# Performance work log

Measured on AMD Instinct MI355X. Metric: run time of the kernel, lower is better.

The kernel has to match this reference:

```python
import jax, jax.numpy as jnp
import numpy as np

B, N, D = 2, 2048, 1536
HEADS, KVH, DQK, DV = 8, 1, 128, 192
G = HEADS // KVH  # query groups per kv head
NP, DP = 512, 128  # pairwise seq len (coarse), pairwise feature dim
SCALE = DQK ** -0.5
CLAMP = 5.0
MOMENTUM = 0.1  # BatchRMSNorm: 1 - 0.9
EPS = 1e-5


def layernorm(x, w, b):
    mu = jnp.mean(x, axis=-1, keepdims=True)
    var = jnp.mean(jnp.square(x - mu), axis=-1, keepdims=True)
    return (x - mu) * jax.lax.rsqrt(var + EPS) * w + b


def setup_inputs() -> dict:
    key = jax.random.key(0)
    ks = jax.random.split(key, 6)
    w = lambda k, shape: jax.random.normal(k, shape, jnp.float32) * 0.02
    return {
        "x": jax.random.normal(ks[0], (B, N, D), jnp.float32),
        "pairwise": jax.random.normal(ks[1], (B, NP, NP, DP), jnp.float32),
        "w_qkv": w(ks[2], (D, HEADS * DQK + KVH * DQK + KVH * DV)),
        "q_w": jnp.ones((DQK,), jnp.float32), "q_b": jnp.zeros((DQK,), jnp.float32),
        "k_w": jnp.ones((DQK,), jnp.float32), "k_b": jnp.zeros((DQK,), jnp.float32),
        "v_w": jnp.ones((DV,), jnp.float32), "v_b": jnp.zeros((DV,), jnp.float32),
        "bias_gamma": jnp.ones((DP,), jnp.float32),
        "bias_beta": jnp.zeros((DP,), jnp.float32),
        "bias_running_var": jnp.ones((DP,), jnp.float32),
        "w_bias": w(ks[3], (DP, HEADS)),
        "w_out": w(ks[4], (HEADS * DV, D)),
        "b_out": jnp.zeros((D,), jnp.float32),
    }


def reference(x, pairwise, w_qkv, q_w, q_b, k_w, k_b, v_w, v_b,
              bias_gamma, bias_beta, bias_running_var, w_bias, w_out, b_out):
    b, n, _ = x.shape
    qkv = x @ w_qkv
    q, k, v = jnp.split(qkv, [HEADS * DQK, HEADS * DQK + KVH * DQK], axis=-1)
    # split heads: q -> b g h n d, k/v -> b h n d
    q = q.reshape(b, n, G, KVH, DQK).transpose(0, 2, 3, 1, 4)
    k = k.reshape(b, n, KVH, DQK).transpose(0, 2, 1, 3)
    v = v.reshape(b, n, KVH, DV).transpose(0, 2, 1, 3)
    q = layernorm(q, q_w, q_b)
    k = layernorm(k, k_w, k_b)
    v = layernorm(v, v_w, v_b)

    sim = jnp.einsum('bghid,bhjd->bghij', q, k) * SCALE

    # BatchRMSNorm (training update of running_var, then normalize)
    flat = pairwise.reshape(-1, DP)
    batch_var = jnp.var(flat, axis=0)  # unbiased=False
    rv = bias_running_var * (1.0 - MOMENTUM) + MOMENTUM * batch_var
    std = jnp.sqrt(rv + EPS)
    normed = pairwise / std * bias_gamma + bias_beta
    bias = jax.nn.gelu(normed, approximate=False) @ w_bias  # b i j (g h)
    bias = bias.reshape(b, NP, NP, G, KVH).transpose(0, 3, 4, 1, 2)  # b g h i j
    r = n // NP  # expand_factor
    bias = jnp.repeat(jnp.repeat(bias, r, axis=-2), r, axis=-1)

    sim = jnp.tanh((sim + bias) / CLAMP) * CLAMP  # softclamp
    attn = jax.nn.softmax(sim, axis=-1)
    out = jnp.einsum('bghij,bhjd->bghid', attn, v)
    out = out.transpose(0, 3, 1, 2, 4).reshape(b, n, HEADS * DV)  # merge heads
    return out @ w_out + b_out
```

## Files before the change

### kernel.cpp

```cpp
#include <hip/hip_runtime.h>
#include <math.h>

typedef _Float16 f16;
typedef unsigned int u32;
typedef __attribute__((ext_vector_type(8))) f16 f16x8;
typedef __attribute__((ext_vector_type(4))) f16 f16x4;
typedef __attribute__((ext_vector_type(4))) float f32x4;
typedef __attribute__((ext_vector_type(16))) float f32x16;

#define DEV static __device__ __forceinline__

#define SEQ 2048
#define DMODEL 1536
#define NHEADS 8
#define DQK 128
#define DVV 192
#define QKVW 1344
#define SCALEQK 0.08838834764831845f
#define LOG2E 1.4426950408889634f

#define OFF_WQKVT 0ull
#define OFF_WOUTT 4128768ull
#define OFF_XH    8847360ull
#define OFF_QKV   21430272ull
#define OFF_Q     43450368ull
#define OFF_K     51838976ull
#define OFF_V     52887552ull
#define OFF_VT    54460416ull
#define OFF_PART  56033280ull
#define OFF_SG    57081856ull
#define OFF_BIASC 57082880ull
#define OFF_AO    65471488ull

DEV float fexp2(float x){
#if __has_builtin(__builtin_amdgcn_exp2f)
  return __builtin_amdgcn_exp2f(x);
#else
  return exp2f(x);
#endif
}
DEV float frcp(float x){
#if __has_builtin(__builtin_amdgcn_rcpf)
  return __builtin_amdgcn_rcpf(x);
#else
  return 1.0f/x;
#endif
}

typedef u32 __attribute__((address_space(1))) u32g;
typedef u32 __attribute__((address_space(3))) u32l;
DEV void g2l16(const void* g, void* l){
  __builtin_amdgcn_global_load_lds((const u32g*)g, (u32l*)l, 16, 0, 0);
}

#define MFMA32(a,b,c) __builtin_amdgcn_mfma_f32_32x32x16_f16(a,b,c,0,0,0)
#define MFMA16(a,b,c) __builtin_amdgcn_mfma_f32_16x16x32_f16(a,b,c,0,0,0)

DEV f32x16 zero16(){
  f32x16 v;
  #pragma unroll
  for (int i=0;i<16;i++) v[i]=0.f;
  return v;
}
DEV f32x4 zero4(){
  f32x4 v;
  #pragma unroll
  for (int i=0;i<4;i++) v[i]=0.f;
  return v;
}

DEV float gelu_f(float x){
  float z  = 0.70710678118654752440f * x;
  float az = fabsf(z);
  float t  = frcp(1.f + 0.3275911f*az);
  float poly = t*(0.254829592f + t*(-0.284496736f + t*(1.421413741f +
               t*(-1.453152027f + t*1.061405429f))));
  float e  = 1.f - poly*fexp2(-z*z*LOG2E);
  float er = (z < 0.f) ? -e : e;
  return 0.5f*x*(1.f + er);
}

__global__ __launch_bounds__(256) void k1_prep(const float* __restrict__ wq, f16* __restrict__ wqT,
                                               const float* __restrict__ wo, f16* __restrict__ woT,
                                               const float* __restrict__ X, f16* __restrict__ Xh){
  __shared__ float t[32][33];
  int bid = blockIdx.x, tid = threadIdx.x;
  if (bid >= 4320){
    size_t i0 = (size_t)(bid - 4320)*2048 + (size_t)tid*8;
    f32x4 a = *(const f32x4*)(X + i0);
    f32x4 b = *(const f32x4*)(X + i0 + 4);
    f16x8 o;
    #pragma unroll
    for (int e=0;e<4;e++){ o[e] = (f16)a[e]; o[4+e] = (f16)b[e]; }
    *(f16x8*)(Xh + i0) = o;
    return;
  }
  int tx = tid & 31, ty = tid >> 5;
  const float* src; f16* dst; int N, x, y;
  if (bid < 2016){ src = wq; dst = wqT; N = 1344; x = bid % 48; y = bid / 48; }
  else { int b2 = bid - 2016; src = wo; dst = woT; N = 1536; x = b2 % 48; y = b2 / 48; }
  int k0 = x*32, n0 = y*32;
  #pragma unroll
  for (int i=0;i<4;i++){ int r = ty+8*i; t[r][tx] = src[(size_t)(k0+r)*N + n0+tx]; }
  __syncthreads();
  #pragma unroll
  for (int i=0;i<4;i++){ int r = ty+8*i; dst[(size_t)(n0+r)*1536 + k0+tx] = (f16)t[tx][r]; }
}

DEV void qkv_body(const f16* __restrict__ A, const f16* __restrict__ WT,
                  float* __restrict__ qkv, char* lds, int bx, int by, int tid){
  int nb = bx*64, mb = by*128;
  int w = tid>>6, lane = tid&63, li = lane&31, h = lane>>5;
  int srow = lane>>3, sc = lane&7;
  f32x16 acc[2]; acc[0]=zero16(); acc[1]=zero16();

#define QG_STAGE(buf, kt_) do { \
    char* ad = lds + (buf)*24576; \
    _Pragma("unroll") \
    for (int s=0;s<4;s++){ \
      int slot = w*4+s; int mlr = slot*8 + srow; int cs = sc ^ (mlr&7); \
      g2l16(A + (size_t)(mb+mlr)*DMODEL + (kt_)*64 + cs*8, ad + slot*1024); \
    } \
    char* bd = lds + (buf)*24576 + 16384; \
    _Pragma("unroll") \
    for (int s=0;s<2;s++){ \
      int slot = w*2+s; int nl = slot*8 + srow; int cs = sc ^ (nl&7); \
      g2l16(WT + (size_t)(nb+nl)*DMODEL + (kt_)*64 + cs*8, bd + slot*1024); \
    } } while(0)

  QG_STAGE(0,0);
  __syncthreads();
  for (int kt=0; kt<24; kt++){
    int cur = kt&1;
    if (kt<23) QG_STAGE(cur^1, kt+1);
    const char* ad = lds + cur*24576;
    const char* bd = lds + cur*24576 + 16384;
    int ml = w*32 + li;
    #pragma unroll
    for (int ks=0; ks<4; ks++){
      f16x8 af = *(const f16x8*)(ad + ml*128 + (((2*ks+h) ^ (ml&7))*16));
      #pragma unroll
      for (int nf=0; nf<2; nf++){
        int nl = nf*32 + li;
        f16x8 bf = *(const f16x8*)(bd + nl*128 + (((2*ks+h) ^ (nl&7))*16));
        acc[nf] = MFMA32(af, bf, acc[nf]);
      }
    }
    __syncthreads();
  }
  #pragma unroll
  for (int nf=0; nf<2; nf++)
    #pragma unroll
    for (int r=0;r<16;r++){
      int m = mb + w*32 + (r&3) + 8*(r>>2) + 4*h;
      int n = nb + nf*32 + li;
      qkv[(size_t)m*QKVW + n] = acc[nf][r];
    }
#undef QG_STAGE
}

DEV void pvar_body(const float* __restrict__ pw, float* __restrict__ partials,
                   char* smem, int id, int tid){
  int q = tid & 31, rg = tid >> 5;
  f32x4 s1 = zero4(), s2 = zero4();
  const float* p0 = pw + ((size_t)id*512 + rg)*128 + q*4;
  #pragma unroll 4
  for (int it=0; it<64; it++){
    f32x4 v = *(const f32x4*)(p0 + (size_t)it*1024);
    s1 += v; s2 += v*v;
  }
  f32x4* r1 = (f32x4*)smem; f32x4* r2 = r1 + 256;
  r1[tid] = s1; r2[tid] = s2;
  __syncthreads();
  if (tid < 64){
    int qq = tid & 31;
    f32x4* rr = (tid >= 32) ? r2 : r1;
    f32x4 a = rr[qq];
    #pragma unroll
    for (int g=1; g<8; g++) a += rr[g*32+qq];
    *(f32x4*)(partials + (size_t)id*256 + ((tid>=32)?128:0) + qq*4) = a;
  }
}

__global__ __launch_bounds__(256,2) void k2_qkv_pvar(const f16* __restrict__ Xh,
    const f16* __restrict__ WT, float* __restrict__ qkv,
    const float* __restrict__ pw, float* __restrict__ partials){
  __shared__ char smem[49152];
  int bid = blockIdx.x, tid = threadIdx.x;
  if (bid < 1536){
    if (bid % 3 == 0){ int qid = bid/3; qkv_body(Xh, WT, qkv, smem, qid%21, qid/21, tid); }
    else { int pid = (bid/3)*2 + (bid%3) - 1; pvar_body(pw, partials, smem, pid, tid); }
  } else {
    int qid = 512 + (bid - 1536);
    qkv_body(Xh, WT, qkv, smem, qid%21, qid/21, tid);
  }
}

DEV void ln_unit(const float* __restrict__ qkv,
    const float* __restrict__ qw, const float* __restrict__ qb,
    const float* __restrict__ kw, const float* __restrict__ kb,
    const float* __restrict__ vw, const float* __restrict__ vb,
    f16* __restrict__ Q, f16* __restrict__ K, f16* __restrict__ V,
    int unit, int lane){
  int row = unit / 10, seg = unit - row*10;
  int b = row >> 11, n = row & 2047;
  const float* base = qkv + (size_t)row*QKVW;
  if (seg < 9){
    int off = seg*128;
    float x0 = base[off+lane], x1 = base[off+64+lane];
    float s = x0+x1;
    #pragma unroll
    for (int d=32; d>=1; d>>=1) s += __shfl_xor(s, d);
    float mu = s*(1.f/128.f);
    float d0 = x0-mu, d1 = x1-mu;
    float vv = d0*d0 + d1*d1;
    #pragma unroll
    for (int d=32; d>=1; d>>=1) vv += __shfl_xor(vv, d);
    float istd = rsqrtf(vv*(1.f/128.f) + 1e-5f);
    const float* W  = (seg<8)? qw : kw;
    const float* Bi = (seg<8)? qb : kb;
    f16* dst = (seg<8) ? (Q + ((size_t)(b*NHEADS+seg)*SEQ + n)*DQK)
                       : (K + ((size_t)(b*SEQ+n))*DQK);
    dst[lane]    = (f16)(d0*istd*W[lane] + Bi[lane]);
    dst[lane+64] = (f16)(d1*istd*W[lane+64] + Bi[lane+64]);
  } else {
    float x0 = base[1152+lane], x1 = base[1152+64+lane], x2 = base[1152+128+lane];
    float s = x0+x1+x2;
    #pragma unroll
    for (int d=32; d>=1; d>>=1) s += __shfl_xor(s, d);
    float mu = s*(1.f/192.f);
    float d0=x0-mu, d1=x1-mu, d2=x2-mu;
    float vv = d0*d0+d1*d1+d2*d2;
    #pragma unroll
    for (int d=32; d>=1; d>>=1) vv += __shfl_xor(vv, d);
    float istd = rsqrtf(vv*(1.f/192.f) + 1e-5f);
    f16* dst = V + (size_t)(b*SEQ+n)*DVV;
    dst[lane]     = (f16)(d0*istd*vw[lane] + vb[lane]);
    dst[lane+64]  = (f16)(d1*istd*vw[lane+64] + vb[lane+64]);
    dst[lane+128] = (f16)(d2*istd*vw[lane+128] + vb[lane+128]);
  }
}

__global__ __launch_bounds__(256,4) void k3_ln_finvar(const float* __restrict__ qkv,
    const float* __restrict__ qw, const float* __restrict__ qb,
    const float* __restrict__ kw, const float* __restrict__ kb,
    const float* __restrict__ vw, const float* __restrict__ vb,
    f16* __restrict__ Q, f16* __restrict__ K, f16* __restrict__ V,
    const float* __restrict__ partials, const float* __restrict__ rvar,
    const float* __restrict__ gamma, const float* __restrict__ beta,
    float* __restrict__ sg, float* __restrict__ sb){
  __shared__ float sh[256];
  int bid = blockIdx.x, tid = threadIdx.x;
  if (bid < 10240){
    ln_unit(qkv, qw,qb,kw,kb,vw,vb, Q,K,V, bid*4 + (tid>>6), tid&63);
  } else {
    int c = tid & 127, wh = tid >> 7;
    float acc = 0.f;
    #pragma unroll 8
    for (int i=0;i<1024;i++) acc += partials[i*256 + wh*128 + c];
    sh[tid] = acc;
    __syncthreads();
    if (tid < 128){
      float s1 = sh[tid], s2 = sh[tid+128];
      const float Minv = 1.f/524288.f;
      float m = s1*Minv;
      float var = s2*Minv - m*m;
      float rv = rvar[tid]*0.9f + 0.1f*var;
      sg[tid] = rsqrtf(rv + 1e-5f)*gamma[tid];
      sb[tid] = beta[tid];
    }
  }
}

DEV void bias_body(const float* __restrict__ pw,
    const float* __restrict__ sg, const float* __restrict__ sb,
    const float* __restrict__ wb, f16* __restrict__ biasc, int bias_id, int tid){
  int w = tid>>6, lane = tid&63;
  int il = lane&15, kg = lane>>4;
  f16x8 bw[4];
  float sgr[32], sbr[32];
  #pragma unroll
  for (int t=0;t<4;t++)
    #pragma unroll
    for (int e=0;e<8;e++){
      int k = t*32 + kg*8 + e;
      bw[t][e] = (f16)((il<8) ? wb[k*8 + il] : 0.f);
      sgr[t*8+e] = sg[k];
      sbr[t*8+e] = sb[k];
    }
  for (int it=0; it<8; it++){
    int tile = bias_id*4 + w + it*4096;
    size_t rg = (size_t)tile*16 + il;
    f32x4 acc = zero4();
    #pragma unroll
    for (int t=0;t<4;t++){
      const float* sp = pw + rg*128 + t*32 + kg*8;
      f32x4 v0 = *(const f32x4*)sp;
      f32x4 v1 = *(const f32x4*)(sp+4);
      f16x8 af;
      #pragma unroll
      for (int e=0;e<4;e++) af[e]   = (f16)gelu_f(v0[e]*sgr[t*8+e]   + sbr[t*8+e]);
      #pragma unroll
      for (int e=0;e<4;e++) af[4+e] = (f16)gelu_f(v1[e]*sgr[t*8+4+e] + sbr[t*8+4+e]);
      acc = MFMA16(af, bw[t], acc);
    }
    if (il < 8){
      #pragma unroll
      for (int r=0;r<4;r++){
        size_t rr = (size_t)tile*16 + kg*4 + r;
        int bb = (int)(rr >> 18);
        int rem = (int)(rr & 262143);
        int ii = rem >> 9, jj = rem & 511;
        biasc[(((size_t)(bb*8 + il)*512) + ii)*512 + jj] = (f16)acc[r];
      }
    }
  }
}

DEV void vtrans_body(const f16* __restrict__ V, f16* __restrict__ VT,
                     f16 (*t)[33], int id, int tid){
  int b = id / 384, rem = id - b*384;
  int d0 = (rem % 6)*32, j0 = (rem / 6)*32;
  int tx = tid & 31, ty = tid >> 5;
  #pragma unroll
  for (int i=0;i<4;i++){ int r = ty+8*i; t[r][tx] = V[((size_t)b*SEQ + j0+r)*DVV + d0+tx]; }
  __syncthreads();
  #pragma unroll
  for (int i=0;i<4;i++){ int r = ty+8*i; VT[((size_t)b*DVV + d0+r)*SEQ + j0+tx] = t[tx][r]; }
}

__global__ __launch_bounds__(256,2) void k4_bias_vtrans(const float* __restrict__ pw,
    const float* __restrict__ sg, const float* __restrict__ sb,
    const float* __restrict__ wb, f16* __restrict__ biasc,
    const f16* __restrict__ V, f16* __restrict__ VT){
  __shared__ f16 tt[32][33];
  int bid = blockIdx.x, tid = threadIdx.x;
  if (bid < 1536){
    if (bid & 1) bias_body(pw, sg, sb, wb, biasc, bid>>1, tid);
    else         vtrans_body(V, VT, tt, bid>>1, tid);
  } else {
    bias_body(pw, sg, sb, wb, biasc, 768 + (bid - 1536), tid);
  }
}

__global__ __launch_bounds__(256,1) void attn(const f16* __restrict__ Q, const f16* __restrict__ K,
                                              const f16* __restrict__ VT, const f16* __restrict__ biasc,
                                              f16* __restrict__ AO){
  __shared__ char lds[81920];
  int bid = blockIdx.x;
  int bg = bid & 15, qt = bid >> 4;
  int b = bg >> 3, g = bg & 7;
  int tid = threadIdx.x;
  int w = tid >> 6, lane = tid & 63;
  int li = lane & 31, h = lane >> 5;

  const f16* Qb = Q  + (size_t)bg*SEQ*DQK;
  const f16* Kb = K  + (size_t)b*SEQ*DQK;
  const f16* Vb = VT + (size_t)b*DVV*SEQ;

  int qrow = qt*128 + w*32 + li;
  f16x8 qf[8];
  #pragma unroll
  for (int ks=0; ks<8; ks++)
    qf[ks] = *(const f16x8*)(Qb + (size_t)qrow*DQK + ks*16 + h*8);

  const f16* brow = biasc + ((size_t)bg*512 + (qrow>>2))*512;

  f32x16 oacc[6];
  #pragma unroll
  for (int nf=0;nf<6;nf++) oacc[nf] = zero16();
  float lsum = 0.f;

  int kl_row = lane >> 4, kl_c = lane & 15;
  int vl_row = lane >> 3, vl_c = lane & 7;

#define STAGE(buf, jt_) do { \
    char* kd = lds + (buf)*40960; \
    const f16* ksrc = Kb + (size_t)(jt_)*64*DQK; \
    _Pragma("unroll") \
    for (int s=0;s<4;s++){ \
      int slot = w*4+s; int jr = slot*4 + kl_row; int cs = kl_c ^ (jr&7); \
      g2l16(ksrc + (size_t)jr*DQK + cs*8, kd + slot*1024); \
    } \
    char* vd = lds + (buf)*40960 + 16384; \
    _Pragma("unroll") \
    for (int s=0;s<6;s++){ \
      int slot = w*6+s; int dvr = slot*8 + vl_row; int cs = vl_c ^ (dvr&7); \
      g2l16(Vb + (size_t)dvr*SEQ + (size_t)(jt_)*64 + cs*8, vd + slot*1024); \
    } } while(0)

  STAGE(0, 0);

  const float CS = SCALEQK * (2.f*LOG2E/5.f);
  const float CB = 2.f*LOG2E/5.f;
  const float CP = 5.f*LOG2E;

  for (int jt=0; jt<32; jt++){
    int cur = jt & 1;
    __syncthreads();
    if (jt < 31) STAGE(cur^1, jt+1);
    const char* kb_ = lds + cur*40960;
    const char* vb_ = lds + cur*40960 + 16384;
    #pragma unroll
    for (int sub=0; sub<2; sub++){
      f32x16 sacc = zero16();
      int jr = sub*32 + li;
      #pragma unroll
      for (int ks=0; ks<8; ks++){
        int ck = (2*ks + h) ^ (jr&7);
        f16x8 kf = *(const f16x8*)(kb_ + jr*256 + ck*16);
        sacc = MFMA32(kf, qf[ks], sacc);
      }
      int jb4 = jt*16 + sub*8;
      f16x8 bv = *(const f16x8*)(brow + jb4);
      float bt[4];
      #pragma unroll
      for (int q=0;q<4;q++){
        float b0 = (float)bv[2*q], b1 = (float)bv[2*q+1];
        bt[q] = (h ? b1 : b0) * CB;
      }
      float p[16], xp[16];
      #pragma unroll
      for (int r=0;r<16;r++){
        float u2 = sacc[r]*CS + bt[r>>2];
        float E  = fexp2(u2);
        float tn = 1.f - 2.f*frcp(E + 1.f);
        float pr = fexp2(tn * CP);
        p[r] = pr;
        lsum += pr;
      }
      #pragma unroll
      for (int r=0;r<16;r++) xp[r] = __shfl_xor(p[r], 32);
      #pragma unroll
      for (int ks2=0; ks2<2; ks2++){
        f16x8 pa;
        #pragma unroll
        for (int e=0;e<4;e++) pa[e] = (f16)(h ? xp[8*ks2+4+e] : p[8*ks2+e]);
        #pragma unroll
        for (int e=4;e<8;e++) pa[e] = (f16)(h ? p[8*ks2+e]    : xp[8*ks2+e-4]);
        #pragma unroll
        for (int nf=0; nf<6; nf++){
          int dvr = nf*32 + li;
          int cj = (sub*4 + 2*ks2 + h) ^ (dvr&7);
          f16x8 vf = *(const f16x8*)(vb_ + dvr*128 + cj*16);
          oacc[nf] = MFMA32(pa, vf, oacc[nf]);
        }
      }
    }
  }
  float ltot = lsum + __shfl_xor(lsum, 32);
  float linv = 1.f / ltot;
  #pragma unroll
  for (int nf=0; nf<6; nf++)
    #pragma unroll
    for (int r=0;r<16;r++){
      int il = (r&3) + 8*(r>>2) + 4*h;
      float ov = oacc[nf][r] * __shfl(linv, il);
      int orow = qt*128 + w*32 + il;
      AO[((size_t)(b*SEQ + orow)*NHEADS + g)*DVV + nf*32 + li] = (f16)ov;
    }
#undef STAGE
}

__global__ __launch_bounds__(256,2) void out_gemm(const f16* __restrict__ A, const f16* __restrict__ WT,
                                                  const float* __restrict__ bo, float* __restrict__ out){
  __shared__ char lds[49152];
  int nb = blockIdx.x*64, mb = blockIdx.y*128;
  int tid = threadIdx.x;
  int w = tid>>6, lane = tid&63, li = lane&31, h = lane>>5;
  int srow = lane>>3, sc = lane&7;
  f32x16 acc[2]; acc[0]=zero16(); acc[1]=zero16();

#define OG_STAGE(buf, kt_) do { \
    char* ad = lds + (buf)*24576; \
    _Pragma("unroll") \
    for (int s=0;s<4;s++){ \
      int slot = w*4+s; int mlr = slot*8 + srow; int cs = sc ^ (mlr&7); \
      g2l16(A + (size_t)(mb+mlr)*DMODEL + (kt_)*64 + cs*8, ad + slot*1024); \
    } \
    char* bd = lds + (buf)*24576 + 16384; \
    _Pragma("unroll") \
    for (int s=0;s<2;s++){ \
      int slot = w*2+s; int nl = slot*8 + srow; int cs = sc ^ (nl&7); \
      g2l16(WT + (size_t)(nb+nl)*DMODEL + (kt_)*64 + cs*8, bd + slot*1024); \
    } } while(0)

  OG_STAGE(0,0);
  __syncthreads();
  for (int kt=0; kt<24; kt++){
    int cur = kt&1;
    if (kt<23) OG_STAGE(cur^1, kt+1);
    const char* ad = lds + cur*24576;
    const char* bd = lds + cur*24576 + 16384;
    int ml = w*32 + li;
    #pragma unroll
    for (int ks=0; ks<4; ks++){
      f16x8 af = *(const f16x8*)(ad + ml*128 + (((2*ks+h) ^ (ml&7))*16));
      #pragma unroll
      for (int nf=0; nf<2; nf++){
        int nl = nf*32 + li;
        f16x8 bf = *(const f16x8*)(bd + nl*128 + (((2*ks+h) ^ (nl&7))*16));
        acc[nf] = MFMA32(af, bf, acc[nf]);
      }
    }
    __syncthreads();
  }
  float bo0 = bo[nb+li], bo1 = bo[nb+32+li];
  #pragma unroll
  for (int nf=0; nf<2; nf++)
    #pragma unroll
    for (int r=0;r<16;r++){
      int m = mb + w*32 + (r&3) + 8*(r>>2) + 4*h;
      int n = nb + nf*32 + li;
      out[(size_t)m*DMODEL + n] = acc[nf][r] + (nf ? bo1 : bo0);
    }
#undef OG_STAGE
}

extern "C" void kernel_launch(void* const* d_in, const int* in_sizes, int n_in,
                              void* d_out, int out_size, void* d_ws, size_t ws_size,
                              hipStream_t stream) {
  (void)in_sizes; (void)n_in; (void)out_size; (void)ws_size;
  const float* x        = (const float*)d_in[0];
  const float* pairwise = (const float*)d_in[1];
  const float* w_qkv    = (const float*)d_in[2];
  const float* q_w      = (const float*)d_in[3];
  const float* q_b      = (const float*)d_in[4];
  const float* k_w      = (const float*)d_in[5];
  const float* k_b      = (const float*)d_in[6];
  const float* v_w      = (const float*)d_in[7];
  const float* v_b      = (const float*)d_in[8];
  const float* bgamma   = (const float*)d_in[9];
  const float* bbeta    = (const float*)d_in[10];
  const float* brvar    = (const float*)d_in[11];
  const float* w_bias   = (const float*)d_in[12];
  const float* w_out    = (const float*)d_in[13];
  const float* b_out    = (const float*)d_in[14];
  float* out = (float*)d_out;

  char* ws = (char*)d_ws;
  f16*   wqkvT = (f16*)(ws + OFF_WQKVT);
  f16*   woutT = (f16*)(ws + OFF_WOUTT);
  f16*   Xh    = (f16*)(ws + OFF_XH);
  float* qkvb  = (float*)(ws + OFF_QKV);
  f16*   Qh    = (f16*)(ws + OFF_Q);
  f16*   Kh    = (f16*)(ws + OFF_K);
  f16*   Vh    = (f16*)(ws + OFF_V);
  f16*   VTh   = (f16*)(ws + OFF_VT);
  float* part  = (float*)(ws + OFF_PART);
  float* sg    = (float*)(ws + OFF_SG);
  float* sb    = sg + 128;
  f16*   biasc = (f16*)(ws + OFF_BIASC);
  f16*   AOh   = (f16*)(ws + OFF_AO);

  k1_prep<<<7392, 256, 0, stream>>>(w_qkv, wqkvT, w_out, woutT, x, Xh);
  k2_qkv_pvar<<<1696, 256, 0, stream>>>(Xh, wqkvT, qkvb, pairwise, part);
  k3_ln_finvar<<<10241, 256, 0, stream>>>(qkvb, q_w,q_b,k_w,k_b,v_w,v_b, Qh, Kh, Vh,
                                          part, brvar, bgamma, bbeta, sg, sb);
  k4_bias_vtrans<<<1792, 256, 0, stream>>>(pairwise, sg, sb, w_bias, biasc, Vh, VTh);
  attn<<<256, 256, 0, stream>>>(Qh, Kh, VTh, biasc, AOh);
  out_gemm<<<dim3(24,32), 256, 0, stream>>>(AOh, woutT, b_out, out);
}
```

Baseline: 351.3 us.

## Enlarge GEMM tiles to 256x64, share one GEMM body, and batch QK MFMAs in attention

Replaces the 128x64 QKV and output GEMM tiles with a shared 256x64 body in which each wave computes a 2x2 grid of 32x32 MFMA tiles, so each LDS fragment load feeds more MFMAs. Block indices are remapped to group tiles, presumably for cache locality, and the QKV/pvar interleave changes to one GEMM block per five. The attention loop now computes both 32-row QK score tiles before the softmax and PV MFMAs, which adds independent MFMA work. The cost is more LDS per block (80KB), which may reduce occupancy, plus higher register pressure from the extra accumulators.

```diff
diff --git a/kernel.cpp b/kernel.cpp
--- a/kernel.cpp
+++ b/kernel.cpp
@@ -107,56 +107,62 @@
   for (int i=0;i<4;i++){ int r = ty+8*i; dst[(size_t)(n0+r)*1536 + k0+tx] = (f16)t[tx][r]; }
 }
 
-DEV void qkv_body(const f16* __restrict__ A, const f16* __restrict__ WT,
-                  float* __restrict__ qkv, char* lds, int bx, int by, int tid){
-  int nb = bx*64, mb = by*128;
+DEV void gemm256_body(const f16* __restrict__ A, const f16* __restrict__ WT,
+                      float* __restrict__ C, int ldc, const float* __restrict__ bo,
+                      char* lds, int bx, int by, int tid){
+  int nb = bx*64, mb = by*256;
   int w = tid>>6, lane = tid&63, li = lane&31, h = lane>>5;
   int srow = lane>>3, sc = lane&7;
-  f32x16 acc[2]; acc[0]=zero16(); acc[1]=zero16();
-
-#define QG_STAGE(buf, kt_) do { \
-    char* ad = lds + (buf)*24576; \
+  f32x16 acc[2][2];
+  acc[0][0]=zero16(); acc[0][1]=zero16(); acc[1][0]=zero16(); acc[1][1]=zero16();
+
+#define G_STAGE(buf, kt_) do { \
+    char* ad = lds + (buf)*40960; \
     _Pragma("unroll") \
-    for (int s=0;s<4;s++){ \
-      int slot = w*4+s; int mlr = slot*8 + srow; int cs = sc ^ (mlr&7); \
+    for (int s=0;s<8;s++){ \
+      int slot = w*8+s; int mlr = slot*8 + srow; int cs = sc ^ (srow&7); \
       g2l16(A + (size_t)(mb+mlr)*DMODEL + (kt_)*64 + cs*8, ad + slot*1024); \
     } \
-    char* bd = lds + (buf)*24576 + 16384; \
+    char* bd = lds + (buf)*40960 + 32768; \
     _Pragma("unroll") \
     for (int s=0;s<2;s++){ \
-      int slot = w*2+s; int nl = slot*8 + srow; int cs = sc ^ (nl&7); \
+      int slot = w*2+s; int nl = slot*8 + srow; int cs = sc ^ (srow&7); \
       g2l16(WT + (size_t)(nb+nl)*DMODEL + (kt_)*64 + cs*8, bd + slot*1024); \
     } } while(0)
 
-  QG_STAGE(0,0);
+  G_STAGE(0,0);
   __syncthreads();
   for (int kt=0; kt<24; kt++){
     int cur = kt&1;
-    if (kt<23) QG_STAGE(cur^1, kt+1);
-    const char* ad = lds + cur*24576;
-    const char* bd = lds + cur*24576 + 16384;
-    int ml = w*32 + li;
+    if (kt<23) G_STAGE(cur^1, kt+1);
+    const char* ad = lds + cur*40960;
+    const char* bd = lds + cur*40960 + 32768;
     #pragma unroll
     for (int ks=0; ks<4; ks++){
-      f16x8 af = *(const f16x8*)(ad + ml*128 + (((2*ks+h) ^ (ml&7))*16));
-      #pragma unroll
-      for (int nf=0; nf<2; nf++){
-        int nl = nf*32 + li;
-        f16x8 bf = *(const f16x8*)(bd + nl*128 + (((2*ks+h) ^ (nl&7))*16));
-        acc[nf] = MFMA32(af, bf, acc[nf]);
+      int cso = ((2*ks+h) ^ (li&7))*16;
+      f16x8 a0 = *(const f16x8*)(ad + (w*64      + li)*128 + cso);
+      f16x8 a1 = *(const f16x8*)(ad + (w*64 + 32 + li)*128 + cso);
+      f16x8 b0 = *(const f16x8*)(bd + (           li)*128 + cso);
+      f16x8 b1 = *(const f16x8*)(bd + (      32 + li)*128 + cso);
+      acc[0][0] = MFMA32(a0, b0, acc[0][0]);
+      acc[0][1] = MFMA32(a0, b1, acc[0][1]);
+      acc[1][0] = MFMA32(a1, b0, acc[1][0]);
+      acc[1][1] = MFMA32(a1, b1, acc[1][1]);
+    }
+    __syncthreads();
+  }
+  float bo0 = bo ? bo[nb+li] : 0.f, bo1 = bo ? bo[nb+32+li] : 0.f;
+  #pragma unroll
+  for (int mi=0; mi<2; mi++)
+    #pragma unroll
+    for (int nf=0; nf<2; nf++)
+      #pragma unroll
+      for (int r=0;r<16;r++){
+        int m = mb + w*64 + mi*32 + (r&3) + 8*(r>>2) + 4*h;
+        int n = nb + nf*32 + li;
+        C[(size_t)m*ldc + n] = acc[mi][nf][r] + (nf ? bo1 : bo0);
       }
-    }
-    __syncthreads();
-  }
-  #pragma unroll
-  for (int nf=0; nf<2; nf++)
-    #pragma unroll
-    for (int r=0;r<16;r++){
-      int m = mb + w*32 + (r&3) + 8*(r>>2) + 4*h;
-      int n = nb + nf*32 + li;
-      qkv[(size_t)m*QKVW + n] = acc[nf][r];
-    }
-#undef QG_STAGE
+#undef G_STAGE
 }
 
 DEV void pvar_body(const float* __restrict__ pw, float* __restrict__ partials,
@@ -185,14 +191,15 @@
 __global__ __launch_bounds__(256,2) void k2_qkv_pvar(const f16* __restrict__ Xh,
     const f16* __restrict__ WT, float* __restrict__ qkv,
     const float* __restrict__ pw, float* __restrict__ partials){
-  __shared__ char smem[49152];
+  __shared__ char smem[81920];
   int bid = blockIdx.x, tid = threadIdx.x;
-  if (bid < 1536){
-    if (bid % 3 == 0){ int qid = bid/3; qkv_body(Xh, WT, qkv, smem, qid%21, qid/21, tid); }
-    else { int pid = (bid/3)*2 + (bid%3) - 1; pvar_body(pw, partials, smem, pid, tid); }
+  if (bid % 5 == 0){
+    int qid = bid/5;
+    int l = (qid&7)*42 + (qid>>3);
+    gemm256_body(Xh, WT, qkv, QKVW, (const float*)0, smem, l%21, l/21, tid);
   } else {
-    int qid = 512 + (bid - 1536);
-    qkv_body(Xh, WT, qkv, smem, qid%21, qid/21, tid);
+    int pid = bid - bid/5 - 1;
+    if (pid < 1024) pvar_body(pw, partials, smem, pid, tid);
   }
 }
 
@@ -401,16 +408,21 @@
     if (jt < 31) STAGE(cur^1, jt+1);
     const char* kb_ = lds + cur*40960;
     const char* vb_ = lds + cur*40960 + 16384;
+
+    f32x16 s0 = zero16(), s1 = zero16();
+    #pragma unroll
+    for (int ks=0; ks<8; ks++){
+      int cso = ((2*ks + h) ^ (li&7))*16;
+      f16x8 kf0 = *(const f16x8*)(kb_ + (     li)*256 + cso);
+      f16x8 kf1 = *(const f16x8*)(kb_ + (32 + li)*256 + cso);
+      s0 = MFMA32(kf0, qf[ks], s0);
+      s1 = MFMA32(kf1, qf[ks], s1);
+    }
+
+    f16x8 pa[2][2];
     #pragma unroll
     for (int sub=0; sub<2; sub++){
-      f32x16 sacc = zero16();
-      int jr = sub*32 + li;
-      #pragma unroll
-      for (int ks=0; ks<8; ks++){
-        int ck = (2*ks + h) ^ (jr&7);
-        f16x8 kf = *(const f16x8*)(kb_ + jr*256 + ck*16);
-        sacc = MFMA32(kf, qf[ks], sacc);
-      }
+      const f32x16& sacc = sub ? s1 : s0;
       int jb4 = jt*16 + sub*8;
       f16x8 bv = *(const f16x8*)(brow + jb4);
       float bt[4];
@@ -433,20 +445,23 @@
       for (int r=0;r<16;r++) xp[r] = __shfl_xor(p[r], 32);
       #pragma unroll
       for (int ks2=0; ks2<2; ks2++){
-        f16x8 pa;
         #pragma unroll
-        for (int e=0;e<4;e++) pa[e] = (f16)(h ? xp[8*ks2+4+e] : p[8*ks2+e]);
+        for (int e=0;e<4;e++) pa[sub][ks2][e] = (f16)(h ? xp[8*ks2+4+e] : p[8*ks2+e]);
         #pragma unroll
-        for (int e=4;e<8;e++) pa[e] = (f16)(h ? p[8*ks2+e]    : xp[8*ks2+e-4]);
+        for (int e=4;e<8;e++) pa[sub][ks2][e] = (f16)(h ? p[8*ks2+e]    : xp[8*ks2+e-4]);
+      }
+    }
+    #pragma unroll
+    for (int sub=0; sub<2; sub++)
+      #pragma unroll
+      for (int ks2=0; ks2<2; ks2++)
         #pragma unroll
         for (int nf=0; nf<6; nf++){
           int dvr = nf*32 + li;
           int cj = (sub*4 + 2*ks2 + h) ^ (dvr&7);
           f16x8 vf = *(const f16x8*)(vb_ + dvr*128 + cj*16);
-          oacc[nf] = MFMA32(pa, vf, oacc[nf]);
+          oacc[nf] = MFMA32(pa[sub][ks2], vf, oacc[nf]);
         }
-      }
-    }
   }
   float ltot = lsum + __shfl_xor(lsum, 32);
   float linv = 1.f / ltot;
@@ -464,57 +479,10 @@
 
 __global__ __launch_bounds__(256,2) void out_gemm(const f16* __restrict__ A, const f16* __restrict__ WT,
                                                   const float* __restrict__ bo, float* __restrict__ out){
-  __shared__ char lds[49152];
-  int nb = blockIdx.x*64, mb = blockIdx.y*128;
-  int tid = threadIdx.x;
-  int w = tid>>6, lane = tid&63, li = lane&31, h = lane>>5;
-  int srow = lane>>3, sc = lane&7;
-  f32x16 acc[2]; acc[0]=zero16(); acc[1]=zero16();
-
-#define OG_STAGE(buf, kt_) do { \
-    char* ad = lds + (buf)*24576; \
-    _Pragma("unroll") \
-    for (int s=0;s<4;s++){ \
-      int slot = w*4+s; int mlr = slot*8 + srow; int cs = sc ^ (mlr&7); \
-      g2l16(A + (size_t)(mb+mlr)*DMODEL + (kt_)*64 + cs*8, ad + slot*1024); \
-    } \
-    char* bd = lds + (buf)*24576 + 16384; \
-    _Pragma("unroll") \
-    for (int s=0;s<2;s++){ \
-      int slot = w*2+s; int nl = slot*8 + srow; int cs = sc ^ (nl&7); \
-      g2l16(WT + (size_t)(nb+nl)*DMODEL + (kt_)*64 + cs*8, bd + slot*1024); \
-    } } while(0)
-
-  OG_STAGE(0,0);
-  __syncthreads();
-  for (int kt=0; kt<24; kt++){
-    int cur = kt&1;
-    if (kt<23) OG_STAGE(cur^1, kt+1);
-    const char* ad = lds + cur*24576;
-    const char* bd = lds + cur*24576 + 16384;
-    int ml = w*32 + li;
-    #pragma unroll
-    for (int ks=0; ks<4; ks++){
-      f16x8 af = *(const f16x8*)(ad + ml*128 + (((2*ks+h) ^ (ml&7))*16));
-      #pragma unroll
-      for (int nf=0; nf<2; nf++){
-        int nl = nf*32 + li;
-        f16x8 bf = *(const f16x8*)(bd + nl*128 + (((2*ks+h) ^ (nl&7))*16));
-        acc[nf] = MFMA32(af, bf, acc[nf]);
-      }
-    }
-    __syncthreads();
-  }
-  float bo0 = bo[nb+li], bo1 = bo[nb+32+li];
-  #pragma unroll
-  for (int nf=0; nf<2; nf++)
-    #pragma unroll
-    for (int r=0;r<16;r++){
-      int m = mb + w*32 + (r&3) + 8*(r>>2) + 4*h;
-      int n = nb + nf*32 + li;
-      out[(size_t)m*DMODEL + n] = acc[nf][r] + (nf ? bo1 : bo0);
-    }
-#undef OG_STAGE
+  __shared__ char lds[81920];
+  int bid = blockIdx.x, tid = threadIdx.x;
+  int l = (bid&7)*48 + (bid>>3);
+  gemm256_body(A, WT, out, DMODEL, bo, lds, l%24, l/24, tid);
 }
 
 extern "C" void kernel_launch(void* const* d_in, const int* in_sizes, int n_in,
@@ -554,10 +522,10 @@
   f16*   AOh   = (f16*)(ws + OFF_AO);
 
   k1_prep<<<7392, 256, 0, stream>>>(w_qkv, wqkvT, w_out, woutT, x, Xh);
-  k2_qkv_pvar<<<1696, 256, 0, stream>>>(Xh, wqkvT, qkvb, pairwise, part);
+  k2_qkv_pvar<<<1680, 256, 0, stream>>>(Xh, wqkvT, qkvb, pairwise, part);
   k3_ln_finvar<<<10241, 256, 0, stream>>>(qkvb, q_w,q_b,k_w,k_b,v_w,v_b, Qh, Kh, Vh,
                                           part, brvar, bgamma, bbeta, sg, sb);
   k4_bias_vtrans<<<1792, 256, 0, stream>>>(pairwise, sg, sb, w_bias, biasc, Vh, VTh);
   attn<<<256, 256, 0, stream>>>(Qh, Kh, VTh, biasc, AOh);
-  out_gemm<<<dim3(24,32), 256, 0, stream>>>(AOh, woutT, b_out, out);
-}
+  out_gemm<<<384, 256, 0, stream>>>(AOh, woutT, b_out, out);
+}
```

New measurement: 358.6 us. 2.1% more time.
